# Optimization experiments

Hardware: AMD Instinct MI355X
Metric: run time of the kernel (lower is better)

## Reference

```python
import jax, jax.numpy as jnp
import numpy as np

B, C, E, H = 8, 2048, 256, 64
N_AGENTS = 4
KAPPA = 0.9
MASKED = True


def _decay_xi_delta(dones):
    """Vectorized equivalent of get_decay_matrix / get_xi / delta.

    dones: [B, C] bool. Timestep dones are dones[:, ::N_AGENTS] -> [B, T].
    The original Python loop builds mask[b,n,m] = exists i with ts_done[b,i]
    and n >= i and m < i, i.e. a done strictly after m and at-or-before n.
    That equals (inclusive_cumsum[n] - inclusive_cumsum[m]) > 0.
    """
    ts = dones[:, ::N_AGENTS]                      # [B, T]
    T = ts.shape[1]
    csum = jnp.cumsum(ts.astype(jnp.int32), axis=1)            # inclusive
    blocked = (csum[:, :, None] - csum[:, None, :]) > 0        # [B, T, T]
    ts_mask = (~blocked).astype(jnp.float32)

    n = jnp.arange(T)
    diff = n[:, None] - n[None, :]
    dm = jnp.where(diff >= 0, KAPPA ** diff.astype(jnp.float32), 0.0)  # [T, T]
    dm = dm[None, :, :] * ts_mask                               # [B, T, T]
    # repeat_interleave over both time axes -> per-agent [B, C, C]
    dm = jnp.repeat(jnp.repeat(dm, N_AGENTS, axis=1), N_AGENTS, axis=2)
    if MASKED:
        Cfull = dm.shape[-1]
        dm = dm * jnp.tril(jnp.ones((Cfull, Cfull), dm.dtype))[None]

    # xi: kappa^(t+1) before the first done, 0 after (per timestep, repeated per agent)
    has_done = jnp.any(ts, axis=1, keepdims=True)               # [B, 1]
    first = jnp.argmax(ts.astype(jnp.float32), axis=1, keepdims=True)
    first = jnp.where(has_done, first, T)                       # [B, 1]
    t_idx = jnp.arange(T)[None, :]                              # [1, T]
    xi = (KAPPA ** (t_idx + 1).astype(jnp.float32)) * (t_idx < first).astype(jnp.float32)
    xi = jnp.repeat(xi, N_AGENTS, axis=1)[:, :, None]           # [B, C, 1]

    delta = (~jnp.any(ts, axis=1)).astype(jnp.float32)[:, None, None]  # [B,1,1]
    return dm, xi, delta


def setup_inputs() -> dict:
    key = jax.random.key(0)
    ks = jax.random.split(key, 8)
    return {
        "key_in": jax.random.normal(ks[0], (B, C, E), jnp.float32),
        "query": jax.random.normal(ks[1], (B, C, E), jnp.float32),
        "value": jax.random.normal(ks[2], (B, C, E), jnp.float32),
        "hstate": jax.random.normal(ks[3], (B, H, H), jnp.float32),
        "dones": jax.random.randint(ks[4], (B, C), 0, 2).astype(bool),
        "w_q": jax.random.normal(ks[5], (E, H), jnp.float32) / np.sqrt(E).astype(np.float32),
        "w_k": jax.random.normal(ks[6], (E, H), jnp.float32) / np.sqrt(E).astype(np.float32),
        "w_v": jax.random.normal(ks[7], (E, H), jnp.float32) / np.sqrt(E).astype(np.float32),
    }


def reference(key_in, query, value, hstate, dones, w_q, w_k, w_v):
    q = query @ w_q                                  # [B, C, H]
    k = key_in @ w_k                                 # [B, C, H]
    v = value @ w_v                                  # [B, C, H]

    dm, xi, delta = _decay_xi_delta(dones)           # [B,C,C], [B,C,1], [B,1,1]
    T = C // N_AGENTS
    chunk_decay = KAPPA ** T

    # next_hstate = k^T @ (v * last_row_of_decay^T) + hstate * chunk_decay * delta
    next_h = jnp.einsum('bch,bcd->bhd', k, v * dm[:, -1, :, None]) \
        + hstate * chunk_decay * delta

    cross = jnp.einsum('bch,bhd->bcd', q, hstate) * xi         # [B, C, H]
    scores = jnp.einsum('bch,bmh->bcm', q, k) * dm              # [B, C, C]
    inner = jnp.einsum('bcm,bmd->bcd', scores, v)               # [B, C, H]
    return inner + cross, next_h
```

## Files before the change

### kernel.cpp

```cpp
#include <hip/hip_runtime.h>
#include <hip/hip_bf16.h>
#include <cstddef>

#define B_ 8
#define C_ 2048
#define E_ 256
#define H_ 64
#define T_ 512
#define NA 4
#define KAPPA 0.9f
#define LOG2_KAPPA (-0.15200309344504997f)
#define KAPPA_T 3.73302e-24f

typedef __attribute__((ext_vector_type(8))) short bf16x8;
typedef __attribute__((ext_vector_type(4))) float f32x4;

__device__ inline short f2bf(float x) {
    unsigned u = __builtin_bit_cast(unsigned, x);
    u += 0x7fff + ((u >> 16) & 1);
    return (short)(u >> 16);
}

__global__ __launch_bounds__(256) void wt_kernel(
    const float* __restrict__ w_q, const float* __restrict__ w_k,
    const float* __restrict__ w_v, short* __restrict__ wt)
{
    const int mat = blockIdx.x >> 2;
    const int k0  = (blockIdx.x & 3) * 64;
    const float* W = (mat == 0) ? w_q : (mat == 1) ? w_k : w_v;
    __shared__ float tile[64][67];
    const int t = threadIdx.x;
#pragma unroll
    for (int pass = 0; pass < 16; ++pass) {
        int idx = pass * 256 + t;
        int r = idx >> 6, c = idx & 63;
        tile[r][c] = W[(size_t)(k0 + r) * H_ + c];
    }
    __syncthreads();
#pragma unroll
    for (int pass = 0; pass < 16; ++pass) {
        int idx = pass * 256 + t;
        int d = idx >> 6, c = idx & 63;
        wt[(size_t)mat * (H_ * E_) + (size_t)d * E_ + k0 + c] = f2bf(tile[c][d]);
    }
}

__global__ __launch_bounds__(256) void proj_mfma(
    const float* __restrict__ key_in, const float* __restrict__ query,
    const float* __restrict__ value, const short* __restrict__ wt,
    float* __restrict__ qp, float* __restrict__ kp, float* __restrict__ vp)
{
    const int mat = blockIdx.y;
    const float* A; float* O;
    if (mat == 0)      { A = query;  O = qp; }
    else if (mat == 1) { A = key_in; O = kp; }
    else               { A = value;  O = vp; }

    __shared__ short Wt[64][264];

    const int t    = threadIdx.x;
    const int b    = blockIdx.x & 7;
    const int rb   = blockIdx.x >> 3;
    const int row0 = b * C_ + rb * 64;
    const int lane = t & 63;
    const int mt   = t >> 6;
    const int lr   = lane & 15;
    const int lg   = lane >> 4;

    const short* wsrc = wt + (size_t)mat * (H_ * E_);
#pragma unroll
    for (int pass = 0; pass < 8; ++pass) {
        int idx = pass * 2048 + t * 8;
        int d = idx >> 8, k = idx & 255;
        *(bf16x8*)&Wt[d][k] = *(const bf16x8*)&wsrc[idx];
    }
    __syncthreads();

    const float* arow = &A[(size_t)(row0 + mt * 16 + lr) * E_ + lg * 8];

    f32x4 acc[4] = {};
#pragma unroll
    for (int kc = 0; kc < 8; ++kc) {
        f32x4 x0 = *(const f32x4*)(arow + kc * 32);
        f32x4 x1 = *(const f32x4*)(arow + kc * 32 + 4);
        bf16x8 af;
        af[0] = f2bf(x0[0]); af[1] = f2bf(x0[1]);
        af[2] = f2bf(x0[2]); af[3] = f2bf(x0[3]);
        af[4] = f2bf(x1[0]); af[5] = f2bf(x1[1]);
        af[6] = f2bf(x1[2]); af[7] = f2bf(x1[3]);
#pragma unroll
        for (int nt = 0; nt < 4; ++nt) {
            bf16x8 bfrag = *(const bf16x8*)&Wt[nt * 16 + lr][kc * 32 + lg * 8];
            acc[nt] = __builtin_amdgcn_mfma_f32_16x16x32_bf16(af, bfrag, acc[nt], 0, 0, 0);
        }
    }

#pragma unroll
    for (int nt = 0; nt < 4; ++nt)
#pragma unroll
        for (int i = 0; i < 4; ++i)
            O[(size_t)(row0 + mt * 16 + lg * 4 + i) * H_ + nt * 16 + lr] = acc[nt][i];
}

__global__ __launch_bounds__(256) void out_kernel(
    const float* __restrict__ qp, const float* __restrict__ kp,
    const float* __restrict__ vp, const float* __restrict__ hs,
    const unsigned char* __restrict__ raw,
    float* __restrict__ out0, float* __restrict__ outh)
{
    const int t    = threadIdx.x;
    const int lane = t & 63;
    const int w    = t >> 6;
    const int bid  = blockIdx.x;

    const uint4* dp = (const uint4*)raw;
    uint4 w0 = dp[lane * 2];
    uint4 w1 = dp[lane * 2 + 1];
    unsigned nz = (w0.x | w0.y | w0.z | w0.w | w1.x | w1.y | w1.z | w1.w) & 0xFFFFFF00u;
    const int stride = (__ballot(nz != 0) != 0ULL) ? 1 : 4;

    if (bid < 1024) {
        const int b = bid & 7;
        const int n = (bid >> 3) * 4 + w;
        const int a = lane >> 4;
        const int g = lane & 15;
        const unsigned char* drow = raw + (size_t)b * C_ * stride;

        int s = 0; bool found = false;
        for (int base = n; ; base -= 64) {
            int j = base - lane;
            unsigned long long m =
                __ballot(j >= 0 && drow[(size_t)(4 * j) * stride] != 0);
            if (m) { s = base - __builtin_ctzll(m); found = true; break; }
            if (base < 64) break;
        }

        const float* kb = kp + (size_t)b * C_ * H_;
        const float* vb = vp + (size_t)b * C_ * H_;
        f32x4 q4 = *(const f32x4*)&qp[((size_t)b * C_ + 4 * n + a) * H_ + 4 * g];

        f32x4 acc = {};
#pragma unroll
        for (int ma = 0; ma < NA; ++ma) {
            const int m = 4 * n + ma;
            f32x4 k4 = *(const f32x4*)&kb[(size_t)m * H_ + 4 * g];
            float p = q4[0] * k4[0] + q4[1] * k4[1] + q4[2] * k4[2] + q4[3] * k4[3];
            p += __shfl_xor(p, 1); p += __shfl_xor(p, 2);
            p += __shfl_xor(p, 4); p += __shfl_xor(p, 8);
            if (ma <= a) {
                f32x4 v4 = *(const f32x4*)&vb[(size_t)m * H_ + 4 * g];
                acc[0] += p * v4[0]; acc[1] += p * v4[1];
                acc[2] += p * v4[2]; acc[3] += p * v4[3];
            }
        }
        float decay = KAPPA;
        for (int mt = n - 1; mt >= s; --mt) {
#pragma unroll
            for (int ma = 0; ma < NA; ++ma) {
                const int m = 4 * mt + ma;
                f32x4 k4 = *(const f32x4*)&kb[(size_t)m * H_ + 4 * g];
                float p = q4[0] * k4[0] + q4[1] * k4[1] + q4[2] * k4[2] + q4[3] * k4[3];
                p += __shfl_xor(p, 1); p += __shfl_xor(p, 2);
                p += __shfl_xor(p, 4); p += __shfl_xor(p, 8);
                p *= decay;
                f32x4 v4 = *(const f32x4*)&vb[(size_t)m * H_ + 4 * g];
                acc[0] += p * v4[0]; acc[1] += p * v4[1];
                acc[2] += p * v4[2]; acc[3] += p * v4[3];
            }
            decay *= KAPPA;
        }
        if (!found) {
            const float xi = exp2f(LOG2_KAPPA * (float)(n + 1));
            const float* hsb = hs + (size_t)b * H_ * H_;
            f32x4 cacc = {};
#pragma unroll
            for (int h = 0; h < H_; ++h) {
                float qh = __shfl(q4[h & 3], (a << 4) + (h >> 2));
                f32x4 h4 = *(const f32x4*)&hsb[h * H_ + 4 * g];
                cacc[0] += qh * h4[0]; cacc[1] += qh * h4[1];
                cacc[2] += qh * h4[2]; cacc[3] += qh * h4[3];
            }
            acc[0] += xi * cacc[0]; acc[1] += xi * cacc[1];
            acc[2] += xi * cacc[2]; acc[3] += xi * cacc[3];
        }
        *(f32x4*)&out0[((size_t)b * C_ + 4 * n + a) * H_ + 4 * g] = acc;
    } else {
        const int j = bid - 1024;
        const int b = j & 7;
        const int h = (j >> 3) * 4 + w;
        const int d = lane;
        const unsigned char* drow = raw + (size_t)b * C_ * stride;

        int s = 0; bool found = false;
        for (int base = T_ - 1; ; base -= 64) {
            int jj = base - lane;
            unsigned long long m =
                __ballot(jj >= 0 && drow[(size_t)(4 * jj) * stride] != 0);
            if (m) { s = base - __builtin_ctzll(m); found = true; break; }
            if (base < 64) break;
        }

        const float* kb = kp + (size_t)b * C_ * H_;
        const float* vb = vp + (size_t)b * C_ * H_;
        float acc = 0.f, wdec = 1.f;
        for (int mt = T_ - 1; mt >= s; --mt) {
#pragma unroll
            for (int ma = 0; ma < NA; ++ma) {
                const int m = 4 * mt + ma;
                acc += wdec * kb[(size_t)m * H_ + h] * vb[(size_t)m * H_ + d];
            }
            wdec *= KAPPA;
        }
        if (!found)
            acc += hs[((size_t)b * H_ + h) * H_ + d] * KAPPA_T;
        outh[((size_t)b * H_ + h) * H_ + d] = acc;
    }
}

extern "C" void kernel_launch(void* const* d_in, const int* in_sizes, int n_in,
                              void* d_out, int out_size, void* d_ws, size_t ws_size,
                              hipStream_t stream)
{
    const float* key_in = (const float*)d_in[0];
    const float* query  = (const float*)d_in[1];
    const float* value  = (const float*)d_in[2];
    const float* hstate = (const float*)d_in[3];
    const unsigned char* dones = (const unsigned char*)d_in[4];
    const float* w_q = (const float*)d_in[5];
    const float* w_k = (const float*)d_in[6];
    const float* w_v = (const float*)d_in[7];

    float* qp = (float*)d_ws;
    float* kp = qp + (size_t)B_ * C_ * H_;
    float* vp = kp + (size_t)B_ * C_ * H_;
    short* wt = (short*)(vp + (size_t)B_ * C_ * H_);

    wt_kernel<<<12, 256, 0, stream>>>(w_q, w_k, w_v, wt);
    dim3 pgrid(B_ * C_ / 64, 3);
    proj_mfma<<<pgrid, 256, 0, stream>>>(key_in, query, value, wt, qp, kp, vp);
    out_kernel<<<1024 + 128, 256, 0, stream>>>(
        qp, kp, vp, hstate, dones,
        (float*)d_out, (float*)d_out + (size_t)B_ * C_ * H_);
}
```

Baseline: 31.31 us.

## Store K/V projections as bf16 and precompute last-done index table

Projected K and V are now written as bf16 instead of fp32, which halves the bytes the output kernel reads in its decay loops and the next-state reduction. The per-row search for the most recent done is moved out of the output kernel into a prep kernel. That kernel builds a per-batch table of last-done indices using ballots, so each wave does a single table load instead of a ballot scan over the done flags. This adds bf16 rounding error on K and V and a larger prep kernel that scans all dones to detect the stride.

```diff
diff --git a/kernel.cpp b/kernel.cpp
--- a/kernel.cpp
+++ b/kernel.cpp
@@ -20,41 +20,93 @@
     u += 0x7fff + ((u >> 16) & 1);
     return (short)(u >> 16);
 }
-
-__global__ __launch_bounds__(256) void wt_kernel(
+__device__ inline float bf2f(unsigned short u) {
+    return __builtin_bit_cast(float, (unsigned)u << 16);
+}
+
+__global__ __launch_bounds__(256) void prep_kernel(
     const float* __restrict__ w_q, const float* __restrict__ w_k,
-    const float* __restrict__ w_v, short* __restrict__ wt)
-{
-    const int mat = blockIdx.x >> 2;
-    const int k0  = (blockIdx.x & 3) * 64;
-    const float* W = (mat == 0) ? w_q : (mat == 1) ? w_k : w_v;
-    __shared__ float tile[64][67];
+    const float* __restrict__ w_v, short* __restrict__ wt,
+    const unsigned char* __restrict__ raw, int* __restrict__ s_tab)
+{
     const int t = threadIdx.x;
-#pragma unroll
-    for (int pass = 0; pass < 16; ++pass) {
-        int idx = pass * 256 + t;
-        int r = idx >> 6, c = idx & 63;
-        tile[r][c] = W[(size_t)(k0 + r) * H_ + c];
-    }
-    __syncthreads();
-#pragma unroll
-    for (int pass = 0; pass < 16; ++pass) {
-        int idx = pass * 256 + t;
-        int d = idx >> 6, c = idx & 63;
-        wt[(size_t)mat * (H_ * E_) + (size_t)d * E_ + k0 + c] = f2bf(tile[c][d]);
+    if (blockIdx.x < 12) {
+        const int mat = blockIdx.x >> 2;
+        const int k0  = (blockIdx.x & 3) * 64;
+        const float* W = (mat == 0) ? w_q : (mat == 1) ? w_k : w_v;
+        __shared__ float tile[64][67];
+#pragma unroll
+        for (int pass = 0; pass < 16; ++pass) {
+            int idx = pass * 256 + t;
+            int r = idx >> 6, c = idx & 63;
+            tile[r][c] = W[(size_t)(k0 + r) * H_ + c];
+        }
+        __syncthreads();
+#pragma unroll
+        for (int pass = 0; pass < 16; ++pass) {
+            int idx = pass * 256 + t;
+            int d = idx >> 6, c = idx & 63;
+            wt[(size_t)mat * (H_ * E_) + (size_t)d * E_ + k0 + c] = f2bf(tile[c][d]);
+        }
+    } else {
+        const int b    = blockIdx.x - 12;
+        const int lane = t & 63;
+        const int w    = t >> 6;
+        __shared__ int f;
+        __shared__ unsigned long long msk[8];
+        if (t == 0) f = 0;
+        __syncthreads();
+        int local = 0;
+        for (int j = t; j < B_ * C_; j += 256)
+            if ((j & 3) && raw[j]) local = 1;
+        if (local) f = 1;
+        __syncthreads();
+        const int stride = f ? 1 : 4;
+        const unsigned char* drow = raw + (size_t)b * C_ * stride;
+
+#pragma unroll
+        for (int cc = 0; cc < 2; ++cc) {
+            const int c = 2 * w + cc;
+            const int n = c * 64 + lane;
+            unsigned long long m =
+                __ballot(drow[(size_t)(4 * n) * stride] != 0);
+            if (lane == 0) msk[c] = m;
+        }
+        __syncthreads();
+#pragma unroll
+        for (int cc = 0; cc < 2; ++cc) {
+            const int c = 2 * w + cc;
+            const int n = c * 64 + lane;
+            unsigned long long lowmask =
+                (lane == 63) ? ~0ULL : ((1ULL << (lane + 1)) - 1ULL);
+            unsigned long long m_le = msk[c] & lowmask;
+            int s = -1;
+            if (m_le) {
+                s = c * 64 + (63 - __builtin_clzll(m_le));
+            } else {
+                for (int c2 = c - 1; c2 >= 0; --c2) {
+                    if (msk[c2]) {
+                        s = c2 * 64 + (63 - __builtin_clzll(msk[c2]));
+                        break;
+                    }
+                }
+            }
+            s_tab[b * T_ + n] = s;
+        }
     }
 }
 
 __global__ __launch_bounds__(256) void proj_mfma(
     const float* __restrict__ key_in, const float* __restrict__ query,
     const float* __restrict__ value, const short* __restrict__ wt,
-    float* __restrict__ qp, float* __restrict__ kp, float* __restrict__ vp)
+    float* __restrict__ qp, unsigned short* __restrict__ kp16,
+    unsigned short* __restrict__ vp16)
 {
     const int mat = blockIdx.y;
-    const float* A; float* O;
-    if (mat == 0)      { A = query;  O = qp; }
-    else if (mat == 1) { A = key_in; O = kp; }
-    else               { A = value;  O = vp; }
+    const float* A;
+    if (mat == 0)      A = query;
+    else if (mat == 1) A = key_in;
+    else               A = value;
 
     __shared__ short Wt[64][264];
 
@@ -95,62 +147,61 @@
         }
     }
 
-#pragma unroll
-    for (int nt = 0; nt < 4; ++nt)
-#pragma unroll
-        for (int i = 0; i < 4; ++i)
-            O[(size_t)(row0 + mt * 16 + lg * 4 + i) * H_ + nt * 16 + lr] = acc[nt][i];
+    if (mat == 0) {
+#pragma unroll
+        for (int nt = 0; nt < 4; ++nt)
+#pragma unroll
+            for (int i = 0; i < 4; ++i)
+                qp[(size_t)(row0 + mt * 16 + lg * 4 + i) * H_ + nt * 16 + lr] =
+                    acc[nt][i];
+    } else {
+        unsigned short* O = (mat == 1) ? kp16 : vp16;
+#pragma unroll
+        for (int nt = 0; nt < 4; ++nt)
+#pragma unroll
+            for (int i = 0; i < 4; ++i)
+                O[(size_t)(row0 + mt * 16 + lg * 4 + i) * H_ + nt * 16 + lr] =
+                    (unsigned short)f2bf(acc[nt][i]);
+    }
 }
 
 __global__ __launch_bounds__(256) void out_kernel(
-    const float* __restrict__ qp, const float* __restrict__ kp,
-    const float* __restrict__ vp, const float* __restrict__ hs,
-    const unsigned char* __restrict__ raw,
+    const float* __restrict__ qp, const unsigned short* __restrict__ kp16,
+    const unsigned short* __restrict__ vp16, const float* __restrict__ hs,
+    const int* __restrict__ s_tab,
     float* __restrict__ out0, float* __restrict__ outh)
 {
     const int t    = threadIdx.x;
     const int lane = t & 63;
     const int w    = t >> 6;
     const int bid  = blockIdx.x;
-
-    const uint4* dp = (const uint4*)raw;
-    uint4 w0 = dp[lane * 2];
-    uint4 w1 = dp[lane * 2 + 1];
-    unsigned nz = (w0.x | w0.y | w0.z | w0.w | w1.x | w1.y | w1.z | w1.w) & 0xFFFFFF00u;
-    const int stride = (__ballot(nz != 0) != 0ULL) ? 1 : 4;
 
     if (bid < 1024) {
         const int b = bid & 7;
         const int n = (bid >> 3) * 4 + w;
         const int a = lane >> 4;
         const int g = lane & 15;
-        const unsigned char* drow = raw + (size_t)b * C_ * stride;
-
-        int s = 0; bool found = false;
-        for (int base = n; ; base -= 64) {
-            int j = base - lane;
-            unsigned long long m =
-                __ballot(j >= 0 && drow[(size_t)(4 * j) * stride] != 0);
-            if (m) { s = base - __builtin_ctzll(m); found = true; break; }
-            if (base < 64) break;
-        }
-
-        const float* kb = kp + (size_t)b * C_ * H_;
-        const float* vb = vp + (size_t)b * C_ * H_;
+
+        const int st = s_tab[b * T_ + n];
+        const int s  = (st < 0) ? 0 : st;
+
+        const unsigned short* kb = kp16 + (size_t)b * C_ * H_;
+        const unsigned short* vb = vp16 + (size_t)b * C_ * H_;
         f32x4 q4 = *(const f32x4*)&qp[((size_t)b * C_ + 4 * n + a) * H_ + 4 * g];
 
         f32x4 acc = {};
 #pragma unroll
         for (int ma = 0; ma < NA; ++ma) {
             const int m = 4 * n + ma;
-            f32x4 k4 = *(const f32x4*)&kb[(size_t)m * H_ + 4 * g];
-            float p = q4[0] * k4[0] + q4[1] * k4[1] + q4[2] * k4[2] + q4[3] * k4[3];
+            ushort4 ku = *(const ushort4*)&kb[(size_t)m * H_ + 4 * g];
+            float p = q4[0] * bf2f(ku.x) + q4[1] * bf2f(ku.y)
+                    + q4[2] * bf2f(ku.z) + q4[3] * bf2f(ku.w);
             p += __shfl_xor(p, 1); p += __shfl_xor(p, 2);
             p += __shfl_xor(p, 4); p += __shfl_xor(p, 8);
             if (ma <= a) {
-                f32x4 v4 = *(const f32x4*)&vb[(size_t)m * H_ + 4 * g];
-                acc[0] += p * v4[0]; acc[1] += p * v4[1];
-                acc[2] += p * v4[2]; acc[3] += p * v4[3];
+                ushort4 vu = *(const ushort4*)&vb[(size_t)m * H_ + 4 * g];
+                acc[0] += p * bf2f(vu.x); acc[1] += p * bf2f(vu.y);
+                acc[2] += p * bf2f(vu.z); acc[3] += p * bf2f(vu.w);
             }
         }
         float decay = KAPPA;
@@ -158,18 +209,19 @@
 #pragma unroll
             for (int ma = 0; ma < NA; ++ma) {
                 const int m = 4 * mt + ma;
-                f32x4 k4 = *(const f32x4*)&kb[(size_t)m * H_ + 4 * g];
-                float p = q4[0] * k4[0] + q4[1] * k4[1] + q4[2] * k4[2] + q4[3] * k4[3];
+                ushort4 ku = *(const ushort4*)&kb[(size_t)m * H_ + 4 * g];
+                float p = q4[0] * bf2f(ku.x) + q4[1] * bf2f(ku.y)
+                        + q4[2] * bf2f(ku.z) + q4[3] * bf2f(ku.w);
                 p += __shfl_xor(p, 1); p += __shfl_xor(p, 2);
                 p += __shfl_xor(p, 4); p += __shfl_xor(p, 8);
                 p *= decay;
-                f32x4 v4 = *(const f32x4*)&vb[(size_t)m * H_ + 4 * g];
-                acc[0] += p * v4[0]; acc[1] += p * v4[1];
-                acc[2] += p * v4[2]; acc[3] += p * v4[3];
+                ushort4 vu = *(const ushort4*)&vb[(size_t)m * H_ + 4 * g];
+                acc[0] += p * bf2f(vu.x); acc[1] += p * bf2f(vu.y);
+                acc[2] += p * bf2f(vu.z); acc[3] += p * bf2f(vu.w);
             }
             decay *= KAPPA;
         }
-        if (!found) {
+        if (st < 0) {
             const float xi = exp2f(LOG2_KAPPA * (float)(n + 1));
             const float* hsb = hs + (size_t)b * H_ * H_;
             f32x4 cacc = {};
@@ -189,29 +241,23 @@
         const int b = j & 7;
         const int h = (j >> 3) * 4 + w;
         const int d = lane;
-        const unsigned char* drow = raw + (size_t)b * C_ * stride;
-
-        int s = 0; bool found = false;
-        for (int base = T_ - 1; ; base -= 64) {
-            int jj = base - lane;
-            unsigned long long m =
-                __ballot(jj >= 0 && drow[(size_t)(4 * jj) * stride] != 0);
-            if (m) { s = base - __builtin_ctzll(m); found = true; break; }
-            if (base < 64) break;
-        }
-
-        const float* kb = kp + (size_t)b * C_ * H_;
-        const float* vb = vp + (size_t)b * C_ * H_;
+
+        const int st = s_tab[b * T_ + (T_ - 1)];
+        const int s  = (st < 0) ? 0 : st;
+
+        const unsigned short* kb = kp16 + (size_t)b * C_ * H_;
+        const unsigned short* vb = vp16 + (size_t)b * C_ * H_;
         float acc = 0.f, wdec = 1.f;
         for (int mt = T_ - 1; mt >= s; --mt) {
 #pragma unroll
             for (int ma = 0; ma < NA; ++ma) {
                 const int m = 4 * mt + ma;
-                acc += wdec * kb[(size_t)m * H_ + h] * vb[(size_t)m * H_ + d];
+                acc += wdec * bf2f(kb[(size_t)m * H_ + h]) *
+                              bf2f(vb[(size_t)m * H_ + d]);
             }
             wdec *= KAPPA;
         }
-        if (!found)
+        if (st < 0)
             acc += hs[((size_t)b * H_ + h) * H_ + d] * KAPPA_T;
         outh[((size_t)b * H_ + h) * H_ + d] = acc;
     }
@@ -230,15 +276,16 @@
     const float* w_k = (const float*)d_in[6];
     const float* w_v = (const float*)d_in[7];
 
-    float* qp = (float*)d_ws;
-    float* kp = qp + (size_t)B_ * C_ * H_;
-    float* vp = kp + (size_t)B_ * C_ * H_;
-    short* wt = (short*)(vp + (size_t)B_ * C_ * H_);
-
-    wt_kernel<<<12, 256, 0, stream>>>(w_q, w_k, w_v, wt);
+    unsigned short* kp16 = (unsigned short*)d_ws;
+    unsigned short* vp16 = kp16 + (size_t)B_ * C_ * H_;
+    float*          qp   = (float*)(vp16 + (size_t)B_ * C_ * H_);
+    short*          wt   = (short*)(qp + (size_t)B_ * C_ * H_);
+    int*            s_tab = (int*)(wt + 3 * H_ * E_);
+
+    prep_kernel<<<20, 256, 0, stream>>>(w_q, w_k, w_v, wt, dones, s_tab);
     dim3 pgrid(B_ * C_ / 64, 3);
-    proj_mfma<<<pgrid, 256, 0, stream>>>(key_in, query, value, wt, qp, kp, vp);
+    proj_mfma<<<pgrid, 256, 0, stream>>>(key_in, query, value, wt, qp, kp16, vp16);
     out_kernel<<<1024 + 128, 256, 0, stream>>>(
-        qp, kp, vp, hstate, dones,
+        qp, kp16, vp16, hstate, s_tab,
         (float*)d_out, (float*)d_out + (size_t)B_ * C_ * H_);
 }
```

Measured after the change: 45.46 us. +45.2%, slower.
